# Performance work log

Hardware: AMD Instinct MI355X
Metric: run time of the kernel (lower is better)

## Reference

```python
import jax, jax.numpy as jnp
import numpy as np

BOX = 32  # uniform ROI crop size (y1-y0 = x1-x0 = 32)


def setup_inputs() -> dict:
    key = jax.random.key(0)
    k1, k2, k3 = jax.random.split(key, 3)
    B, C, H, W = 8, 256, 200, 200
    N = 512
    feature_map = jax.random.normal(k1, (B, C, H, W), dtype=jnp.float32)
    boxes_yx = jax.random.randint(k2, (N, 2), 0, H - BOX, dtype=jnp.int32)  # top-left (y0, x0)
    assoc = jax.random.randint(k3, (N,), 0, B, dtype=jnp.int32)            # sample index per box
    return {"feature_map": feature_map, "boxes_yx": boxes_yx, "assoc": assoc}


def reference(feature_map, boxes_yx, assoc):
    # Faithful RoiCut: for each box i, crop feature_map[assoc[i], :, y0:y0+BOX, x0:x0+BOX].
    # clip_boxes=True -> clip box coords into the scene extent.
    B, C, H, W = feature_map.shape
    yx = jnp.clip(boxes_yx, 0, jnp.array([H - BOX, W - BOX], dtype=boxes_yx.dtype))

    def crop(a, yx_i):
        fm = feature_map[a]  # [C, H, W] gather of the associated sample
        return jax.lax.dynamic_slice(fm, (jnp.int32(0), yx_i[0], yx_i[1]), (C, BOX, BOX))

    box_features = jax.vmap(crop)(assoc, yx)  # [N, C, BOX, BOX]
    return box_features
```

## Files before the change

### kernel.cpp

```cpp
#include <hip/hip_runtime.h>


typedef float v4f __attribute__((ext_vector_type(4)));

constexpr int C_     = 256;
constexpr int H_     = 200;
constexpr int W_     = 200;
constexpr int BOX_   = 32;
constexpr int N_     = 512;
constexpr int B_     = 8;
constexpr int PLANE  = H_ * W_;
constexpr int QROWS  = 50;
constexpr int NQ     = 4;
constexpr int NBIN   = B_ * NQ;
constexpr int QLDS   = QROWS * W_;
constexpr int QLDS4  = QLDS / 4;

__global__ __launch_bounds__(512) void group_boxes_kernel(
    const int* __restrict__ boxes,
    const int* __restrict__ assoc,
    unsigned int* __restrict__ keys,
    int* __restrict__ starts)
{
    __shared__ int cnt[NBIN];
    __shared__ int base[NBIN + 1];
    int t = threadIdx.x;

    if (t < NBIN) cnt[t] = 0;
    __syncthreads();

    int y0 = boxes[2 * t];
    int x0 = boxes[2 * t + 1];
    y0 = min(max(y0, 0), H_ - BOX_);
    x0 = min(max(x0, 0), W_ - BOX_);
    int a = assoc[t];
    unsigned int key = ((unsigned int)y0 << 17) | ((unsigned int)x0 << 9) | (unsigned int)t;

    int q0 = y0 / QROWS;
    int q1 = (y0 + BOX_ - 1) / QROWS;
    int bin0 = a * NQ + q0;
    int p0 = atomicAdd(&cnt[bin0], 1);
    int bin1 = -1, p1 = -1;
    if (q1 != q0) {
        bin1 = a * NQ + q1;
        p1 = atomicAdd(&cnt[bin1], 1);
    }
    __syncthreads();

    if (t == 0) {
        int s = 0;
        for (int i = 0; i < NBIN; ++i) { base[i] = s; s += cnt[i]; }
        base[NBIN] = s;
    }
    __syncthreads();

    keys[base[bin0] + p0] = key;
    if (p1 >= 0) keys[base[bin1] + p1] = key;
    if (t <= NBIN) starts[t] = base[t];
}

__global__ __launch_bounds__(512, 8) void roicut_kernel(
    const float* __restrict__ fm,
    const unsigned int* __restrict__ keys,
    const int* __restrict__ starts,
    float* __restrict__ out)
{
    __shared__ float lds[QLDS];

    int bid = blockIdx.x;
    int qtr = bid & 3;
    int c   = (bid >> 2) & 255;
    int a   = bid >> 10;
    int t   = threadIdx.x;

    int bin = a * NQ + qtr;
    int b0 = starts[bin], b1 = starts[bin + 1];
    if (b0 == b1) return;

    const v4f* src = (const v4f*)(fm + (size_t)(a * C_ + c) * PLANE) + qtr * QLDS4;
    v4f* l4 = (v4f*)lds;
    v4f r0 = src[t];
    v4f r1 = src[t + 512];
    v4f r2 = src[t + 1024];
    v4f r3 = src[t + 1536];
    bool tail = t < (QLDS4 - 2048);
    v4f r4;
    if (tail) r4 = src[t + 2048];
    l4[t]        = r0;
    l4[t + 512]  = r1;
    l4[t + 1024] = r2;
    l4[t + 1536] = r3;
    if (tail) l4[t + 2048] = r4;
    __syncthreads();

    int sub   = t >> 8;
    int q     = t & 255;
    int y     = q >> 3;
    int xg    = (q & 7) << 2;
    int rbase = qtr * QROWS;

    for (int b = b0; b < b1; b += 2) {
        int bb = b + sub;
        if (bb < b1) {
            unsigned int v = keys[bb];
            int y0 = (v >> 17) & 255;
            int x0 = (v >> 9) & 255;
            int i  = (int)(v & 511u);
            int ly = y0 + y - rbase;
            if (ly >= 0 && ly < QROWS) {
                const float* p = lds + ly * W_ + (x0 + xg);
                v4f vv;
                vv[0] = p[0]; vv[1] = p[1]; vv[2] = p[2]; vv[3] = p[3];
                v4f* dst = (v4f*)(out + (((size_t)i << 18) + ((size_t)c << 10) + (size_t)(q << 2)));
                __builtin_nontemporal_store(vv, dst);
            }
        }
    }
}

extern "C" void kernel_launch(void* const* d_in, const int* in_sizes, int n_in,
                              void* d_out, int out_size, void* d_ws, size_t ws_size,
                              hipStream_t stream) {
    const float* fm    = (const float*)d_in[0];
    const int*   boxes = (const int*)d_in[1];
    const int*   assoc = (const int*)d_in[2];
    float*       out   = (float*)d_out;

    unsigned int* keys   = (unsigned int*)d_ws;
    int*          starts = (int*)d_ws + 2 * N_;

    group_boxes_kernel<<<1, N_, 0, stream>>>(boxes, assoc, keys, starts);

    int grid = B_ * C_ * NQ;
    roicut_kernel<<<grid, 512, 0, stream>>>(fm, keys, starts, out);
}
```

Baseline: 180.6 us.

## Double-buffer plane quarters via direct global-to-LDS loads per channel block

Each block now handles a whole channel plane rather than one quarter of it. The four quarters are staged through two LDS buffers with global_load_lds, so loading the next quarter overlaps cropping from the current one. The grid shrinks fourfold, and the LDS reads use a per-row element rotation to spread bank accesses. The risks are less parallelism and occupancy from fewer blocks with larger dynamic LDS, and that empty quarters are no longer skipped before being loaded.

Result: no change. 181.6 us (+0.5%).

```diff
diff --git a/kernel.cpp b/kernel.cpp
--- a/kernel.cpp
+++ b/kernel.cpp
@@ -13,8 +13,8 @@
 constexpr int QROWS  = 50;
 constexpr int NQ     = 4;
 constexpr int NBIN   = B_ * NQ;
-constexpr int QLDS   = QROWS * W_;
-constexpr int QLDS4  = QLDS / 4;
+constexpr int QFLT   = QROWS * W_;
+constexpr int BUFFLT = 10240;
 
 __global__ __launch_bounds__(512) void group_boxes_kernel(
     const int* __restrict__ boxes,
@@ -59,60 +59,97 @@
     if (t <= NBIN) starts[t] = base[t];
 }
 
-__global__ __launch_bounds__(512, 8) void roicut_kernel(
+static __device__ __forceinline__ void gload16(const float* g, float* l) {
+    __builtin_amdgcn_global_load_lds(
+        (const __attribute__((address_space(1))) void*)g,
+        (__attribute__((address_space(3))) void*)l,
+        16, 0, 0);
+}
+
+__global__ __launch_bounds__(512) void roicut_kernel(
     const float* __restrict__ fm,
     const unsigned int* __restrict__ keys,
     const int* __restrict__ starts,
     float* __restrict__ out)
 {
-    __shared__ float lds[QLDS];
+    extern __shared__ float lds[];
 
-    int bid = blockIdx.x;
-    int qtr = bid & 3;
-    int c   = (bid >> 2) & 255;
-    int a   = bid >> 10;
-    int t   = threadIdx.x;
+    int bid  = blockIdx.x;
+    int c    = bid & 255;
+    int a    = bid >> 8;
+    int t    = threadIdx.x;
+    int w    = t >> 6;
+    int lane = t & 63;
 
-    int bin = a * NQ + qtr;
-    int b0 = starts[bin], b1 = starts[bin + 1];
-    if (b0 == b1) return;
+    const float* plane = fm + (size_t)(a * C_ + c) * PLANE;
 
-    const v4f* src = (const v4f*)(fm + (size_t)(a * C_ + c) * PLANE) + qtr * QLDS4;
-    v4f* l4 = (v4f*)lds;
-    v4f r0 = src[t];
-    v4f r1 = src[t + 512];
-    v4f r2 = src[t + 1024];
-    v4f r3 = src[t + 1536];
-    bool tail = t < (QLDS4 - 2048);
-    v4f r4;
-    if (tail) r4 = src[t + 2048];
-    l4[t]        = r0;
-    l4[t + 512]  = r1;
-    l4[t + 1024] = r2;
-    l4[t + 1536] = r3;
-    if (tail) l4[t + 2048] = r4;
-    __syncthreads();
+    int segf = w * 1280;
+    int lo4  = lane * 4;
 
-    int sub   = t >> 8;
-    int q     = t & 255;
-    int y     = q >> 3;
-    int xg    = (q & 7) << 2;
-    int rbase = qtr * QROWS;
+    auto stage = [&](int q, int buf) {
+        const float* qb = plane + q * QFLT;
+        float*       lb = lds + buf * BUFFLT;
+        if (w < 7) {
+            #pragma unroll
+            for (int i = 0; i < 5; ++i)
+                gload16(qb + segf + i * 256 + lo4, lb + segf + i * 256);
+        } else {
+            #pragma unroll
+            for (int i = 0; i < 4; ++i)
+                gload16(qb + segf + i * 256 + lo4, lb + segf + i * 256);
+            int off = lo4 > 12 ? 12 : lo4;
+            gload16(qb + 9984 + off, lb + 9984);
+        }
+    };
 
-    for (int b = b0; b < b1; b += 2) {
-        int bb = b + sub;
-        if (bb < b1) {
-            unsigned int v = keys[bb];
-            int y0 = (v >> 17) & 255;
-            int x0 = (v >> 9) & 255;
-            int i  = (int)(v & 511u);
-            int ly = y0 + y - rbase;
-            if (ly >= 0 && ly < QROWS) {
-                const float* p = lds + ly * W_ + (x0 + xg);
-                v4f vv;
-                vv[0] = p[0]; vv[1] = p[1]; vv[2] = p[2]; vv[3] = p[3];
-                v4f* dst = (v4f*)(out + (((size_t)i << 18) + ((size_t)c << 10) + (size_t)(q << 2)));
-                __builtin_nontemporal_store(vv, dst);
+    int sub = t >> 8;
+    int q   = t & 255;
+    int y   = q >> 3;
+    int xg  = (q & 7) << 2;
+    int rot = y & 3;
+
+    stage(0, 0);
+
+    for (int k = 0; k < NQ; ++k) {
+        __builtin_amdgcn_sched_barrier(0);
+        __builtin_amdgcn_s_barrier();
+
+        if (k < NQ - 1) {
+            stage(k + 1, (k + 1) & 1);
+            asm volatile("s_waitcnt vmcnt(5)" ::: "memory");
+        } else {
+            asm volatile("s_waitcnt vmcnt(0)" ::: "memory");
+        }
+        __builtin_amdgcn_sched_barrier(0);
+        __builtin_amdgcn_s_barrier();
+
+        int bin = a * NQ + k;
+        int b0 = starts[bin], b1 = starts[bin + 1];
+        const float* lb = lds + (k & 1) * BUFFLT;
+        int rbase = k * QROWS;
+
+        for (int b = b0; b < b1; b += 2) {
+            int bb = b + sub;
+            if (bb < b1) {
+                unsigned int v = keys[bb];
+                int y0 = (v >> 17) & 255;
+                int x0 = (v >> 9) & 255;
+                int i  = (int)(v & 511u);
+                int ly = y0 + y - rbase;
+                if (ly >= 0 && ly < QROWS) {
+                    const float* p = lb + ly * W_ + (x0 + xg);
+                    v4f vv;
+                    vv[0] = p[0 ^ rot];
+                    vv[1] = p[1 ^ rot];
+                    vv[2] = p[2 ^ rot];
+                    vv[3] = p[3 ^ rot];
+                    v4f s1 = { vv[1], vv[0], vv[3], vv[2] };
+                    vv = (rot & 1) ? s1 : vv;
+                    v4f s2 = { vv[2], vv[3], vv[0], vv[1] };
+                    vv = (rot & 2) ? s2 : vv;
+                    v4f* dst = (v4f*)(out + (((size_t)i << 18) + ((size_t)c << 10) + (size_t)(q << 2)));
+                    __builtin_nontemporal_store(vv, dst);
+                }
             }
         }
     }
@@ -129,8 +166,12 @@
     unsigned int* keys   = (unsigned int*)d_ws;
     int*          starts = (int*)d_ws + 2 * N_;
 
+    (void)hipFuncSetAttribute((const void*)roicut_kernel,
+                              hipFuncAttributeMaxDynamicSharedMemorySize,
+                              2 * BUFFLT * (int)sizeof(float));
+
     group_boxes_kernel<<<1, N_, 0, stream>>>(boxes, assoc, keys, starts);
 
-    int grid = B_ * C_ * NQ;
-    roicut_kernel<<<grid, 512, 0, stream>>>(fm, keys, starts, out);
+    int grid = B_ * C_;
+    roicut_kernel<<<grid, 512, 2 * BUFFLT * sizeof(float), stream>>>(fm, keys, starts, out);
 }
```
